# Kernel tuning notes

Hardware: AMD Instinct MI355X
Metric: run time of the kernel (lower is better)

The kernel has to match this reference:

```python
import jax, jax.numpy as jnp
import numpy as np

N = 20000      # number of nodes
K = 32         # neighbors per node (per edge type)
D_FEAT = 128   # feature dim


def setup_inputs() -> dict:
    key = jax.random.key(0)
    k1, k2, k3 = jax.random.split(key, 3)
    feat = jax.random.normal(k1, (N, D_FEAT), dtype=jnp.float32)
    sim_idx = jax.random.randint(k2, (N, K), 0, N)
    cor_idx = jax.random.randint(k3, (N, K), 0, N)
    return {"feat": feat, "sim_idx": sim_idx, "cor_idx": cor_idx}


def _coattention(Dm, Qm):
    # Dm, Qm: [N, K, d]
    L = jnp.einsum('nkd,njd->nkj', Dm, Qm)          # [N, K, K]
    AC = jax.nn.softmax(L, axis=-1)                  # softmax over Q-neighbors
    AS = jax.nn.softmax(jnp.swapaxes(L, 1, 2), axis=-1)  # softmax over D-neighbors
    CQ = jnp.einsum('nkj,njd->nkd', AC, Qm)          # [N, K, d]
    CD = jnp.einsum('nkj,njd->nkd', AS, jnp.concatenate([Dm, CQ], axis=-1))  # [N, K, 2d]
    return jnp.concatenate([Qm, CD], axis=-1)        # [N, K, 3d]


def reference(feat, sim_idx, cor_idx):
    # mode == 'cor': D <- sim edges, Q <- cor edges (dropout=0 => identity)
    Dm = feat[sim_idx]   # [N, K, d] gather
    Qm = feat[cor_idx]   # [N, K, d] gather
    h = _coattention(Dm, Qm)                          # [N, K, 3d]
    n, k, td = h.shape
    # AvgPool1d(kernel=3, stride=3) over last dim -> [N, K, d]
    h = h.reshape(n, k, td // 3, 3).mean(axis=-1)
    h_neigh = h.mean(axis=1)                          # mean over K neighbors -> [N, d]
    return feat + h_neigh
```

## Files before the change

### kernel.cpp

```cpp
#include <hip/hip_runtime.h>

#define KN 32
#define DF 128
#define WPB 2

typedef float  f32x16 __attribute__((ext_vector_type(16)));
typedef float  f32x2  __attribute__((ext_vector_type(2)));
typedef short  s16x8  __attribute__((ext_vector_type(8)));

union ldsu { int4 i; s16x8 v; };

__device__ __forceinline__ unsigned int pk_bf16(float lo, float hi) {
    unsigned int r;
    asm("v_cvt_pk_bf16_f32 %0, %1, %2" : "=v"(r) : "v"(lo), "v"(hi));
    return r;
}

__device__ __forceinline__ void gll16(const void* g, void* l) {
    __builtin_amdgcn_global_load_lds(
        (const __attribute__((address_space(1))) unsigned int*)g,
        (__attribute__((address_space(3))) unsigned int*)l,
        16, 0, 0);
}

__global__ __launch_bounds__(256)
void cvt_kernel(const float* __restrict__ f, unsigned short* __restrict__ bf,
                unsigned char* __restrict__ f8, int n8) {
    const int i = blockIdx.x * blockDim.x + threadIdx.x;
    if (i >= n8) return;
    float4 x0 = ((const float4*)f)[2 * i];
    float4 x1 = ((const float4*)f)[2 * i + 1];
    int4 b;
    b.x = (int)pk_bf16(x0.x, x0.y); b.y = (int)pk_bf16(x0.z, x0.w);
    b.z = (int)pk_bf16(x1.x, x1.y); b.w = (int)pk_bf16(x1.z, x1.w);
    ((int4*)bf)[i] = b;
    int p0 = __builtin_amdgcn_cvt_pk_fp8_f32(x0.x, x0.y, 0, false);
    p0     = __builtin_amdgcn_cvt_pk_fp8_f32(x0.z, x0.w, p0, true);
    int p1 = __builtin_amdgcn_cvt_pk_fp8_f32(x1.x, x1.y, 0, false);
    p1     = __builtin_amdgcn_cvt_pk_fp8_f32(x1.z, x1.w, p1, true);
    ((int2*)f8)[i] = make_int2(p0, p1);
}

__global__ __launch_bounds__(WPB * 64, 2)
void coattn_kernel(const float* __restrict__ feat,
                   const unsigned char* __restrict__ featbf,
                   const unsigned char* __restrict__ feat8,
                   const int* __restrict__ sim_idx,
                   const int* __restrict__ cor_idx,
                   float* __restrict__ out, int nnodes) {
    __shared__ int4 Ls[WPB][KN][8];
    const int wv = threadIdx.x >> 6;
    const int l  = threadIdx.x & 63;
    const int c  = l & 31;
    const int h  = l >> 5;
    const int g  = l >> 3;
    const int m  = l & 7;
    const int n  = blockIdx.x * WPB + wv;
    if (n >= nnodes) return;

    const int si = sim_idx[n * KN + c];
    const int ci = cor_idx[n * KN + c];
    const unsigned swz = (unsigned)(((m ^ g) & 7) * 16);

    f32x16 acc  = {0,0,0,0,0,0,0,0,0,0,0,0,0,0,0,0};
    f32x16 accT = {0,0,0,0,0,0,0,0,0,0,0,0,0,0,0,0};
    #pragma unroll
    for (int H = 0; H < 2; ++H) {
        const unsigned hoff = (unsigned)(H * 128) + swz;
        #pragma unroll
        for (int t = 0; t < 4; ++t) {
            const unsigned rD = (unsigned)__shfl(si, 8 * t + g, 64);
            gll16(featbf + rD * 256u + hoff, (void*)&Ls[wv][8 * t][0]);
        }
        asm volatile("s_waitcnt vmcnt(0)" ::: "memory");
        __builtin_amdgcn_sched_barrier(0);
        s16x8 fD[4];
        #pragma unroll
        for (int sp = 0; sp < 4; ++sp) {
            union ldsu u; u.i = Ls[wv][c][(sp * 2 + h) ^ (c & 7)];
            fD[sp] = u.v;
        }
        asm volatile("s_waitcnt lgkmcnt(0)" ::: "memory");
        __builtin_amdgcn_sched_barrier(0);
        #pragma unroll
        for (int t = 0; t < 4; ++t) {
            const unsigned rQ = (unsigned)__shfl(ci, 8 * t + g, 64);
            gll16(featbf + rQ * 256u + hoff, (void*)&Ls[wv][8 * t][0]);
        }
        asm volatile("s_waitcnt vmcnt(0)" ::: "memory");
        __builtin_amdgcn_sched_barrier(0);
        #pragma unroll
        for (int sp = 0; sp < 4; ++sp) {
            union ldsu uQ; uQ.i = Ls[wv][c][(sp * 2 + h) ^ (c & 7)];
            acc  = __builtin_amdgcn_mfma_f32_32x32x16_bf16(fD[sp], uQ.v, acc,  0, 0, 0);
            accT = __builtin_amdgcn_mfma_f32_32x32x16_bf16(uQ.v, fD[sp], accT, 0, 0, 0);
        }
        asm volatile("s_waitcnt lgkmcnt(0)" ::: "memory");
        __builtin_amdgcn_sched_barrier(0);
    }

    float mx = acc[0];
    #pragma unroll
    for (int p = 1; p < 16; ++p) mx = fmaxf(mx, acc[p]);
    mx = fmaxf(mx, __shfl_xor(mx, 32, 64));
    float z = 0.f;
    #pragma unroll
    for (int p = 0; p < 16; ++p) z += __expf(acc[p] - mx);
    z += __shfl_xor(z, 32, 64);
    const float invZ = 1.0f / z;

    float rm = accT[0];
    #pragma unroll
    for (int p = 1; p < 16; ++p) rm = fmaxf(rm, accT[p]);
    rm = fmaxf(rm, __shfl_xor(rm, 32, 64));
    float rs = 0.f;
    #pragma unroll
    for (int p = 0; p < 16; ++p) rs += __expf(accT[p] - rm);
    rs += __shfl_xor(rs, 32, 64);
    const float invR = 1.0f / rs;

    float w = 0.f;
    #pragma unroll
    for (int p = 0; p < 16; ++p) {
        const int jp = (p & 3) + 8 * (p >> 2) + 4 * h;
        w += __expf(accT[p] - __shfl(mx, jp, 64)) * __shfl(invZ, jp, 64);
    }
    w += __shfl_xor(w, 32, 64);

    const float u = w * invR;
    float v = 0.f;
    #pragma unroll
    for (int p = 0; p < 16; ++p) {
        const int kp = (p & 3) + 8 * (p >> 2) + 4 * h;
        v += __expf(acc[p] - __shfl(rm, kp, 64)) * __shfl(u, kp, 64);
    }
    v += __shfl_xor(v, 32, 64);

    float sQ[4] = {0,0,0,0}, sD[4] = {0,0,0,0}, sC[4] = {0,0,0,0};
    #pragma unroll
    for (int t = 0; t < 16; ++t) {
        const int b = h * 16 + t;
        const unsigned rD = (unsigned)__shfl(si, b, 64);
        const unsigned rQ = (unsigned)__shfl(ci, b, 64);
        const float wb = __shfl(w, b, 64);
        const float vb = __shfl(v, b, 64);
        const unsigned int da = *(const unsigned int*)(feat8 + (rD << 7) + 4u * c);
        const unsigned int dq = *(const unsigned int*)(feat8 + (rQ << 7) + 4u * c);
        f32x2 a01 = __builtin_amdgcn_cvt_pk_f32_fp8((int)da, false);
        f32x2 a23 = __builtin_amdgcn_cvt_pk_f32_fp8((int)da, true);
        f32x2 q01 = __builtin_amdgcn_cvt_pk_f32_fp8((int)dq, false);
        f32x2 q23 = __builtin_amdgcn_cvt_pk_f32_fp8((int)dq, true);
        sQ[0] += q01[0]; sQ[1] += q01[1]; sQ[2] += q23[0]; sQ[3] += q23[1];
        sD[0] = fmaf(wb, a01[0], sD[0]); sD[1] = fmaf(wb, a01[1], sD[1]);
        sD[2] = fmaf(wb, a23[0], sD[2]); sD[3] = fmaf(wb, a23[1], sD[3]);
        sC[0] = fmaf(vb, q01[0], sC[0]); sC[1] = fmaf(vb, q01[1], sC[1]);
        sC[2] = fmaf(vb, q23[0], sC[2]); sC[3] = fmaf(vb, q23[1], sC[3]);
    }
    #pragma unroll
    for (int i = 0; i < 4; ++i) {
        sQ[i] += __shfl_xor(sQ[i], 32, 64);
        sD[i] += __shfl_xor(sD[i], 32, 64);
        sC[i] += __shfl_xor(sC[i], 32, 64);
    }

    float* const S_sh = (float*)Ls[wv];
    if (h == 0) {
        *(float4*)&S_sh[0 * DF + 4 * c] = make_float4(sQ[0], sQ[1], sQ[2], sQ[3]);
        *(float4*)&S_sh[1 * DF + 4 * c] = make_float4(sD[0], sD[1], sD[2], sD[3]);
        *(float4*)&S_sh[2 * DF + 4 * c] = make_float4(sC[0], sC[1], sC[2], sC[3]);
    }
    asm volatile("s_waitcnt lgkmcnt(0)" ::: "memory");
    const float h0 = S_sh[6 * l + 0] + S_sh[6 * l + 1] + S_sh[6 * l + 2];
    const float h1 = S_sh[6 * l + 3] + S_sh[6 * l + 4] + S_sh[6 * l + 5];
    const float* fr = feat + (long)n * DF;
    const float o0 = fr[2 * l + 0] + h0 * (1.0f / 96.0f);
    const float o1 = fr[2 * l + 1] + h1 * (1.0f / 96.0f);
    *(float2*)&out[(long)n * DF + 2 * l] = make_float2(o0, o1);
}

#define RP 136
__global__ __launch_bounds__(64, 2)
void coattn_v4(const float* __restrict__ feat,
               const int* __restrict__ sim_idx,
               const int* __restrict__ cor_idx,
               float* __restrict__ out, int nnodes) {
    __shared__ unsigned char lds[2 * KN * RP];
    unsigned char* Ab8 = lds;
    unsigned char* Bb8 = lds + KN * RP;
    float* S_sh = (float*)lds;
    const int n = blockIdx.x;
    const int l = threadIdx.x;
    const int c = l & 31;
    const int h = l >> 5;
    const int si = sim_idx[n * KN + c];
    const int ci = cor_idx[n * KN + c];
    const float* Dr = feat + (long)si * DF;
    const float* Qr = feat + (long)ci * DF;
    f32x16 acc  = {0,0,0,0,0,0,0,0,0,0,0,0,0,0,0,0};
    f32x16 accT = {0,0,0,0,0,0,0,0,0,0,0,0,0,0,0,0};
    #pragma unroll
    for (int s = 0; s < 8; ++s) {
        const int d0 = s * 16 + h * 8;
        float4 a0 = *(const float4*)(Dr + d0);
        float4 a1 = *(const float4*)(Dr + d0 + 4);
        float4 b0 = *(const float4*)(Qr + d0);
        float4 b1 = *(const float4*)(Qr + d0 + 4);
        union { s16x8 v8; unsigned int u[4]; } ua, ub;
        ua.u[0] = pk_bf16(a0.x, a0.y); ua.u[1] = pk_bf16(a0.z, a0.w);
        ua.u[2] = pk_bf16(a1.x, a1.y); ua.u[3] = pk_bf16(a1.z, a1.w);
        ub.u[0] = pk_bf16(b0.x, b0.y); ub.u[1] = pk_bf16(b0.z, b0.w);
        ub.u[2] = pk_bf16(b1.x, b1.y); ub.u[3] = pk_bf16(b1.z, b1.w);
        acc  = __builtin_amdgcn_mfma_f32_32x32x16_bf16(ua.v8, ub.v8, acc,  0, 0, 0);
        accT = __builtin_amdgcn_mfma_f32_32x32x16_bf16(ub.v8, ua.v8, accT, 0, 0, 0);
        int pa0 = __builtin_amdgcn_cvt_pk_fp8_f32(a0.x, a0.y, 0, false);
        pa0     = __builtin_amdgcn_cvt_pk_fp8_f32(a0.z, a0.w, pa0, true);
        int pa1 = __builtin_amdgcn_cvt_pk_fp8_f32(a1.x, a1.y, 0, false);
        pa1     = __builtin_amdgcn_cvt_pk_fp8_f32(a1.z, a1.w, pa1, true);
        int pb0 = __builtin_amdgcn_cvt_pk_fp8_f32(b0.x, b0.y, 0, false);
        pb0     = __builtin_amdgcn_cvt_pk_fp8_f32(b0.z, b0.w, pb0, true);
        int pb1 = __builtin_amdgcn_cvt_pk_fp8_f32(b1.x, b1.y, 0, false);
        pb1     = __builtin_amdgcn_cvt_pk_fp8_f32(b1.z, b1.w, pb1, true);
        *(int2*)(Ab8 + c * RP + d0) = make_int2(pa0, pa1);
        *(int2*)(Bb8 + c * RP + d0) = make_int2(pb0, pb1);
    }
    float mx = acc[0];
    #pragma unroll
    for (int p = 1; p < 16; ++p) mx = fmaxf(mx, acc[p]);
    mx = fmaxf(mx, __shfl_xor(mx, 32, 64));
    float z = 0.f;
    #pragma unroll
    for (int p = 0; p < 16; ++p) z += __expf(acc[p] - mx);
    z += __shfl_xor(z, 32, 64);
    const float invZ = 1.0f / z;
    float rm = accT[0];
    #pragma unroll
    for (int p = 1; p < 16; ++p) rm = fmaxf(rm, accT[p]);
    rm = fmaxf(rm, __shfl_xor(rm, 32, 64));
    float rs = 0.f;
    #pragma unroll
    for (int p = 0; p < 16; ++p) rs += __expf(accT[p] - rm);
    rs += __shfl_xor(rs, 32, 64);
    const float invR = 1.0f / rs;
    float w = 0.f;
    #pragma unroll
    for (int p = 0; p < 16; ++p) {
        const int jp = (p & 3) + 8 * (p >> 2) + 4 * h;
        w += __expf(accT[p] - __shfl(mx, jp, 64)) * __shfl(invZ, jp, 64);
    }
    w += __shfl_xor(w, 32, 64);
    const float u = w * invR;
    float v = 0.f;
    #pragma unroll
    for (int p = 0; p < 16; ++p) {
        const int kp = (p & 3) + 8 * (p >> 2) + 4 * h;
        v += __expf(acc[p] - __shfl(rm, kp, 64)) * __shfl(u, kp, 64);
    }
    v += __shfl_xor(v, 32, 64);
    __syncthreads();
    float sQ[4] = {0,0,0,0}, sD[4] = {0,0,0,0}, sC[4] = {0,0,0,0};
    const unsigned char* Abase = Ab8 + h * 16 * RP + 4 * c;
    const unsigned char* Bbase = Bb8 + h * 16 * RP + 4 * c;
    #pragma unroll
    for (int t = 0; t < 16; ++t) {
        const int b = h * 16 + t;
        const float wb = __shfl(w, b, 64);
        const float vb = __shfl(v, b, 64);
        const unsigned int da = *(const unsigned int*)(Abase + t * RP);
        const unsigned int dq = *(const unsigned int*)(Bbase + t * RP);
        f32x2 a01 = __builtin_amdgcn_cvt_pk_f32_fp8((int)da, false);
        f32x2 a23 = __builtin_amdgcn_cvt_pk_f32_fp8((int)da, true);
        f32x2 q01 = __builtin_amdgcn_cvt_pk_f32_fp8((int)dq, false);
        f32x2 q23 = __builtin_amdgcn_cvt_pk_f32_fp8((int)dq, true);
        sQ[0] += q01[0]; sQ[1] += q01[1]; sQ[2] += q23[0]; sQ[3] += q23[1];
        sD[0] = fmaf(wb, a01[0], sD[0]); sD[1] = fmaf(wb, a01[1], sD[1]);
        sD[2] = fmaf(wb, a23[0], sD[2]); sD[3] = fmaf(wb, a23[1], sD[3]);
        sC[0] = fmaf(vb, q01[0], sC[0]); sC[1] = fmaf(vb, q01[1], sC[1]);
        sC[2] = fmaf(vb, q23[0], sC[2]);
        sC[3] = fmaf(vb, q23[1], sC[3]);
    }
    #pragma unroll
    for (int i = 0; i < 4; ++i) {
        sQ[i] += __shfl_xor(sQ[i], 32, 64);
        sD[i] += __shfl_xor(sD[i], 32, 64);
        sC[i] += __shfl_xor(sC[i], 32, 64);
    }
    __syncthreads();
    if (h == 0) {
        *(float4*)&S_sh[0 * DF + 4 * c] = make_float4(sQ[0], sQ[1], sQ[2], sQ[3]);
        *(float4*)&S_sh[1 * DF + 4 * c] = make_float4(sD[0], sD[1], sD[2], sD[3]);
        *(float4*)&S_sh[2 * DF + 4 * c] = make_float4(sC[0], sC[1], sC[2], sC[3]);
    }
    __syncthreads();
    const float h0 = S_sh[6 * l + 0] + S_sh[6 * l + 1] + S_sh[6 * l + 2];
    const float h1 = S_sh[6 * l + 3] + S_sh[6 * l + 4] + S_sh[6 * l + 5];
    const float* fr = feat + (long)n * DF;
    const float o0 = fr[2 * l + 0] + h0 * (1.0f / 96.0f);
    const float o1 = fr[2 * l + 1] + h1 * (1.0f / 96.0f);
    *(float2*)&out[(long)n * DF + 2 * l] = make_float2(o0, o1);
}

extern "C" void kernel_launch(void* const* d_in, const int* in_sizes, int n_in,
                              void* d_out, int out_size, void* d_ws, size_t ws_size,
                              hipStream_t stream) {
    const float* feat = (const float*)d_in[0];
    const int* sim    = (const int*)d_in[1];
    const int* cor    = (const int*)d_in[2];
    float* out        = (float*)d_out;
    const int nnodes  = in_sizes[0] / DF;
    const size_t nfeat = (size_t)nnodes * DF;
    const size_t need  = nfeat * 2 + nfeat;

    if (ws_size >= need) {
        unsigned short* featbf = (unsigned short*)d_ws;
        unsigned char*  feat8  = (unsigned char*)d_ws + nfeat * 2;
        const int n8 = (int)(nfeat / 8);
        hipLaunchKernelGGL(cvt_kernel, dim3((n8 + 255) / 256), dim3(256), 0, stream,
                           feat, featbf, feat8, n8);
        const int blocks = (nnodes + WPB - 1) / WPB;
        hipLaunchKernelGGL(coattn_kernel, dim3(blocks), dim3(WPB * 64), 0, stream,
                           feat, (const unsigned char*)featbf, feat8, sim, cor, out, nnodes);
    } else {
        hipLaunchKernelGGL(coattn_v4, dim3(nnodes), dim3(64), 0, stream,
                           feat, sim, cor, out, nnodes);
    }
}
```

Before: 61.91 us.

## Overlap D/Q and fp8 gathers with MFMA, fold log2e into bf16 scaling

The co-attention kernel now issues the D and Q bf16 gathers for both halves into separate LDS buffers, so the second half's loads and all fp8 row gathers for the final aggregation are in flight while the first half's MFMAs run. Fine-grained vmcnt waits replace the full drains that were needed before. The bf16 features are pre-scaled by sqrt(log2 e), so the MFMA logits come out in base-2 and the softmax can use raw v_exp_f32 instead of __expf. The aggregation FMAs are rewritten with 2-wide vectors to encourage packed math. The hand-counted vmcnt values and the extra registers held for 32 prefetched dwords add fragility and may raise register pressure.

```diff
diff --git a/kernel.cpp b/kernel.cpp
--- a/kernel.cpp
+++ b/kernel.cpp
@@ -15,7 +15,9 @@
     asm("v_cvt_pk_bf16_f32 %0, %1, %2" : "=v"(r) : "v"(lo), "v"(hi));
     return r;
 }
-
+__device__ __forceinline__ float ex2(float x) {
+    float r; asm("v_exp_f32 %0, %1" : "=v"(r) : "v"(x)); return r;
+}
 __device__ __forceinline__ void gll16(const void* g, void* l) {
     __builtin_amdgcn_global_load_lds(
         (const __attribute__((address_space(1))) unsigned int*)g,
@@ -28,11 +30,12 @@
                 unsigned char* __restrict__ f8, int n8) {
     const int i = blockIdx.x * blockDim.x + threadIdx.x;
     if (i >= n8) return;
+    const float s = 1.20112240872f;
     float4 x0 = ((const float4*)f)[2 * i];
     float4 x1 = ((const float4*)f)[2 * i + 1];
     int4 b;
-    b.x = (int)pk_bf16(x0.x, x0.y); b.y = (int)pk_bf16(x0.z, x0.w);
-    b.z = (int)pk_bf16(x1.x, x1.y); b.w = (int)pk_bf16(x1.z, x1.w);
+    b.x = (int)pk_bf16(s * x0.x, s * x0.y); b.y = (int)pk_bf16(s * x0.z, s * x0.w);
+    b.z = (int)pk_bf16(s * x1.x, s * x1.y); b.w = (int)pk_bf16(s * x1.z, s * x1.w);
     ((int4*)bf)[i] = b;
     int p0 = __builtin_amdgcn_cvt_pk_fp8_f32(x0.x, x0.y, 0, false);
     p0     = __builtin_amdgcn_cvt_pk_fp8_f32(x0.z, x0.w, p0, true);
@@ -48,7 +51,7 @@
                    const int* __restrict__ sim_idx,
                    const int* __restrict__ cor_idx,
                    float* __restrict__ out, int nnodes) {
-    __shared__ int4 Ls[WPB][KN][8];
+    __shared__ int4 Ls[WPB][2][KN][8];
     const int wv = threadIdx.x >> 6;
     const int l  = threadIdx.x & 63;
     const int c  = l & 31;
@@ -62,41 +65,79 @@
     const int ci = cor_idx[n * KN + c];
     const unsigned swz = (unsigned)(((m ^ g) & 7) * 16);
 
+    #pragma unroll
+    for (int t = 0; t < 4; ++t) {
+        const unsigned rD = (unsigned)__shfl(si, 8 * t + g, 64);
+        gll16(featbf + rD * 256u + swz, (void*)&Ls[wv][0][8 * t][0]);
+    }
+    #pragma unroll
+    for (int t = 0; t < 4; ++t) {
+        const unsigned rQ = (unsigned)__shfl(ci, 8 * t + g, 64);
+        gll16(featbf + rQ * 256u + swz, (void*)&Ls[wv][1][8 * t][0]);
+    }
+    asm volatile("s_waitcnt vmcnt(4)" ::: "memory");
+    __builtin_amdgcn_sched_barrier(0);
+    s16x8 fD[4], fQ[4];
+    #pragma unroll
+    for (int sp = 0; sp < 4; ++sp) {
+        union ldsu u; u.i = Ls[wv][0][c][(sp * 2 + h) ^ (c & 7)]; fD[sp] = u.v;
+    }
+    asm volatile("s_waitcnt vmcnt(0)" ::: "memory");
+    __builtin_amdgcn_sched_barrier(0);
+    #pragma unroll
+    for (int sp = 0; sp < 4; ++sp) {
+        union ldsu u; u.i = Ls[wv][1][c][(sp * 2 + h) ^ (c & 7)]; fQ[sp] = u.v;
+    }
+    asm volatile("s_waitcnt lgkmcnt(0)" ::: "memory");
+    __builtin_amdgcn_sched_barrier(0);
+
+    #pragma unroll
+    for (int t = 0; t < 4; ++t) {
+        const unsigned rD = (unsigned)__shfl(si, 8 * t + g, 64);
+        gll16(featbf + rD * 256u + 128u + swz, (void*)&Ls[wv][0][8 * t][0]);
+    }
+    #pragma unroll
+    for (int t = 0; t < 4; ++t) {
+        const unsigned rQ = (unsigned)__shfl(ci, 8 * t + g, 64);
+        gll16(featbf + rQ * 256u + 128u + swz, (void*)&Ls[wv][1][8 * t][0]);
+    }
+    unsigned int da[16], dq[16];
+    #pragma unroll
+    for (int t = 0; t < 16; ++t) {
+        const unsigned rD = (unsigned)__shfl(si, h * 16 + t, 64);
+        const unsigned rQ = (unsigned)__shfl(ci, h * 16 + t, 64);
+        const unsigned char* pD = feat8 + (rD << 7) + 4u * c;
+        const unsigned char* pQ = feat8 + (rQ << 7) + 4u * c;
+        asm volatile("global_load_dword %0, %1, off" : "=v"(da[t]) : "v"(pD) : "memory");
+        asm volatile("global_load_dword %0, %1, off" : "=v"(dq[t]) : "v"(pQ) : "memory");
+    }
+
     f32x16 acc  = {0,0,0,0,0,0,0,0,0,0,0,0,0,0,0,0};
     f32x16 accT = {0,0,0,0,0,0,0,0,0,0,0,0,0,0,0,0};
     #pragma unroll
-    for (int H = 0; H < 2; ++H) {
-        const unsigned hoff = (unsigned)(H * 128) + swz;
-        #pragma unroll
-        for (int t = 0; t < 4; ++t) {
-            const unsigned rD = (unsigned)__shfl(si, 8 * t + g, 64);
-            gll16(featbf + rD * 256u + hoff, (void*)&Ls[wv][8 * t][0]);
-        }
-        asm volatile("s_waitcnt vmcnt(0)" ::: "memory");
-        __builtin_amdgcn_sched_barrier(0);
-        s16x8 fD[4];
-        #pragma unroll
-        for (int sp = 0; sp < 4; ++sp) {
-            union ldsu u; u.i = Ls[wv][c][(sp * 2 + h) ^ (c & 7)];
-            fD[sp] = u.v;
-        }
-        asm volatile("s_waitcnt lgkmcnt(0)" ::: "memory");
-        __builtin_amdgcn_sched_barrier(0);
-        #pragma unroll
-        for (int t = 0; t < 4; ++t) {
-            const unsigned rQ = (unsigned)__shfl(ci, 8 * t + g, 64);
-            gll16(featbf + rQ * 256u + hoff, (void*)&Ls[wv][8 * t][0]);
-        }
-        asm volatile("s_waitcnt vmcnt(0)" ::: "memory");
-        __builtin_amdgcn_sched_barrier(0);
-        #pragma unroll
-        for (int sp = 0; sp < 4; ++sp) {
-            union ldsu uQ; uQ.i = Ls[wv][c][(sp * 2 + h) ^ (c & 7)];
-            acc  = __builtin_amdgcn_mfma_f32_32x32x16_bf16(fD[sp], uQ.v, acc,  0, 0, 0);
-            accT = __builtin_amdgcn_mfma_f32_32x32x16_bf16(uQ.v, fD[sp], accT, 0, 0, 0);
-        }
-        asm volatile("s_waitcnt lgkmcnt(0)" ::: "memory");
-        __builtin_amdgcn_sched_barrier(0);
+    for (int sp = 0; sp < 4; ++sp) {
+        acc  = __builtin_amdgcn_mfma_f32_32x32x16_bf16(fD[sp], fQ[sp], acc,  0, 0, 0);
+        accT = __builtin_amdgcn_mfma_f32_32x32x16_bf16(fQ[sp], fD[sp], accT, 0, 0, 0);
+    }
+
+    asm volatile("s_waitcnt vmcnt(36)" ::: "memory");
+    __builtin_amdgcn_sched_barrier(0);
+    #pragma unroll
+    for (int sp = 0; sp < 4; ++sp) {
+        union ldsu u; u.i = Ls[wv][0][c][(sp * 2 + h) ^ (c & 7)]; fD[sp] = u.v;
+    }
+    asm volatile("s_waitcnt vmcnt(32)" ::: "memory");
+    __builtin_amdgcn_sched_barrier(0);
+    #pragma unroll
+    for (int sp = 0; sp < 4; ++sp) {
+        union ldsu u; u.i = Ls[wv][1][c][(sp * 2 + h) ^ (c & 7)]; fQ[sp] = u.v;
+    }
+    asm volatile("s_waitcnt lgkmcnt(0)" ::: "memory");
+    __builtin_amdgcn_sched_barrier(0);
+    #pragma unroll
+    for (int sp = 0; sp < 4; ++sp) {
+        acc  = __builtin_amdgcn_mfma_f32_32x32x16_bf16(fD[sp], fQ[sp], acc,  0, 0, 0);
+        accT = __builtin_amdgcn_mfma_f32_32x32x16_bf16(fQ[sp], fD[sp], accT, 0, 0, 0);
     }
 
     float mx = acc[0];
@@ -105,7 +146,7 @@
     mx = fmaxf(mx, __shfl_xor(mx, 32, 64));
     float z = 0.f;
     #pragma unroll
-    for (int p = 0; p < 16; ++p) z += __expf(acc[p] - mx);
+    for (int p = 0; p < 16; ++p) z += ex2(acc[p] - mx);
     z += __shfl_xor(z, 32, 64);
     const float invZ = 1.0f / z;
 
@@ -115,7 +156,7 @@
     rm = fmaxf(rm, __shfl_xor(rm, 32, 64));
     float rs = 0.f;
     #pragma unroll
-    for (int p = 0; p < 16; ++p) rs += __expf(accT[p] - rm);
+    for (int p = 0; p < 16; ++p) rs += ex2(accT[p] - rm);
     rs += __shfl_xor(rs, 32, 64);
     const float invR = 1.0f / rs;
 
@@ -123,7 +164,7 @@
     #pragma unroll
     for (int p = 0; p < 16; ++p) {
         const int jp = (p & 3) + 8 * (p >> 2) + 4 * h;
-        w += __expf(accT[p] - __shfl(mx, jp, 64)) * __shfl(invZ, jp, 64);
+        w += ex2(accT[p] - __shfl(mx, jp, 64)) * __shfl(invZ, jp, 64);
     }
     w += __shfl_xor(w, 32, 64);
 
@@ -132,42 +173,42 @@
     #pragma unroll
     for (int p = 0; p < 16; ++p) {
         const int kp = (p & 3) + 8 * (p >> 2) + 4 * h;
-        v += __expf(acc[p] - __shfl(rm, kp, 64)) * __shfl(u, kp, 64);
+        v += ex2(acc[p] - __shfl(rm, kp, 64)) * __shfl(u, kp, 64);
     }
     v += __shfl_xor(v, 32, 64);
 
-    float sQ[4] = {0,0,0,0}, sD[4] = {0,0,0,0}, sC[4] = {0,0,0,0};
+    asm volatile("s_waitcnt vmcnt(0)" ::: "memory");
+    __builtin_amdgcn_sched_barrier(0);
+    f32x2 sQ2[2] = {{0.f,0.f},{0.f,0.f}};
+    f32x2 sD2[2] = {{0.f,0.f},{0.f,0.f}};
+    f32x2 sC2[2] = {{0.f,0.f},{0.f,0.f}};
     #pragma unroll
     for (int t = 0; t < 16; ++t) {
         const int b = h * 16 + t;
-        const unsigned rD = (unsigned)__shfl(si, b, 64);
-        const unsigned rQ = (unsigned)__shfl(ci, b, 64);
         const float wb = __shfl(w, b, 64);
         const float vb = __shfl(v, b, 64);
-        const unsigned int da = *(const unsigned int*)(feat8 + (rD << 7) + 4u * c);
-        const unsigned int dq = *(const unsigned int*)(feat8 + (rQ << 7) + 4u * c);
-        f32x2 a01 = __builtin_amdgcn_cvt_pk_f32_fp8((int)da, false);
-        f32x2 a23 = __builtin_amdgcn_cvt_pk_f32_fp8((int)da, true);
-        f32x2 q01 = __builtin_amdgcn_cvt_pk_f32_fp8((int)dq, false);
-        f32x2 q23 = __builtin_amdgcn_cvt_pk_f32_fp8((int)dq, true);
-        sQ[0] += q01[0]; sQ[1] += q01[1]; sQ[2] += q23[0]; sQ[3] += q23[1];
-        sD[0] = fmaf(wb, a01[0], sD[0]); sD[1] = fmaf(wb, a01[1], sD[1]);
-        sD[2] = fmaf(wb, a23[0], sD[2]); sD[3] = fmaf(wb, a23[1], sD[3]);
-        sC[0] = fmaf(vb, q01[0], sC[0]); sC[1] = fmaf(vb, q01[1], sC[1]);
-        sC[2] = fmaf(vb, q23[0], sC[2]); sC[3] = fmaf(vb, q23[1], sC[3]);
-    }
-    #pragma unroll
-    for (int i = 0; i < 4; ++i) {
-        sQ[i] += __shfl_xor(sQ[i], 32, 64);
-        sD[i] += __shfl_xor(sD[i], 32, 64);
-        sC[i] += __shfl_xor(sC[i], 32, 64);
+        f32x2 a01 = __builtin_amdgcn_cvt_pk_f32_fp8((int)da[t], false);
+        f32x2 a23 = __builtin_amdgcn_cvt_pk_f32_fp8((int)da[t], true);
+        f32x2 q01 = __builtin_amdgcn_cvt_pk_f32_fp8((int)dq[t], false);
+        f32x2 q23 = __builtin_amdgcn_cvt_pk_f32_fp8((int)dq[t], true);
+        const f32x2 wb2 = {wb, wb};
+        const f32x2 vb2 = {vb, vb};
+        sQ2[0] += q01;                sQ2[1] += q23;
+        sD2[0] = wb2 * a01 + sD2[0];  sD2[1] = wb2 * a23 + sD2[1];
+        sC2[0] = vb2 * q01 + sC2[0];  sC2[1] = vb2 * q23 + sC2[1];
+    }
+    #pragma unroll
+    for (int i = 0; i < 2; ++i) {
+        sQ2[i][0] += __shfl_xor(sQ2[i][0], 32, 64); sQ2[i][1] += __shfl_xor(sQ2[i][1], 32, 64);
+        sD2[i][0] += __shfl_xor(sD2[i][0], 32, 64); sD2[i][1] += __shfl_xor(sD2[i][1], 32, 64);
+        sC2[i][0] += __shfl_xor(sC2[i][0], 32, 64); sC2[i][1] += __shfl_xor(sC2[i][1], 32, 64);
     }
 
     float* const S_sh = (float*)Ls[wv];
     if (h == 0) {
-        *(float4*)&S_sh[0 * DF + 4 * c] = make_float4(sQ[0], sQ[1], sQ[2], sQ[3]);
-        *(float4*)&S_sh[1 * DF + 4 * c] = make_float4(sD[0], sD[1], sD[2], sD[3]);
-        *(float4*)&S_sh[2 * DF + 4 * c] = make_float4(sC[0], sC[1], sC[2], sC[3]);
+        *(float4*)&S_sh[0 * DF + 4 * c] = make_float4(sQ2[0][0], sQ2[0][1], sQ2[1][0], sQ2[1][1]);
+        *(float4*)&S_sh[1 * DF + 4 * c] = make_float4(sD2[0][0], sD2[0][1], sD2[1][0], sD2[1][1]);
+        *(float4*)&S_sh[2 * DF + 4 * c] = make_float4(sC2[0][0], sC2[0][1], sC2[1][0], sC2[1][1]);
     }
     asm volatile("s_waitcnt lgkmcnt(0)" ::: "memory");
     const float h0 = S_sh[6 * l + 0] + S_sh[6 * l + 1] + S_sh[6 * l + 2];
```

Measured after the change: 63.99 us. 3.4% more time.

## Reuse staged bf16 rows for pooling, prefetch all halves, fold log2e into scaling

Applied to the files above, without the earlier changes.

The conversion kernel now writes only a bf16 copy, pre-scaled by sqrt(log2 e), so the raw v_exp_f32 base-2 instruction can compute softmax exponentials directly. The coattention kernel issues all four D/Q half-row gathers into a larger LDS buffer up front, so the second half's loads overlap the first half's MFMAs. The weighted neighbor sums then read the bf16 rows already in LDS instead of doing a second global gather of an fp8 copy. Output is rescaled by 1/s to compensate. The cost is four times the LDS per block and the extra scaling multiplies.

```diff
diff --git a/kernel.cpp b/kernel.cpp
--- a/kernel.cpp
+++ b/kernel.cpp
@@ -5,7 +5,6 @@
 #define WPB 2
 
 typedef float  f32x16 __attribute__((ext_vector_type(16)));
-typedef float  f32x2  __attribute__((ext_vector_type(2)));
 typedef short  s16x8  __attribute__((ext_vector_type(8)));
 
 union ldsu { int4 i; s16x8 v; };
@@ -15,6 +14,11 @@
     asm("v_cvt_pk_bf16_f32 %0, %1, %2" : "=v"(r) : "v"(lo), "v"(hi));
     return r;
 }
+__device__ __forceinline__ float ex2(float x) {
+    float r; asm("v_exp_f32 %0, %1" : "=v"(r) : "v"(x)); return r;
+}
+__device__ __forceinline__ float bflo(unsigned int u) { return __uint_as_float(u << 16); }
+__device__ __forceinline__ float bfhi(unsigned int u) { return __uint_as_float(u & 0xffff0000u); }
 
 __device__ __forceinline__ void gll16(const void* g, void* l) {
     __builtin_amdgcn_global_load_lds(
@@ -24,31 +28,25 @@
 }
 
 __global__ __launch_bounds__(256)
-void cvt_kernel(const float* __restrict__ f, unsigned short* __restrict__ bf,
-                unsigned char* __restrict__ f8, int n8) {
+void cvt_kernel(const float* __restrict__ f, unsigned short* __restrict__ bf, int n8) {
     const int i = blockIdx.x * blockDim.x + threadIdx.x;
     if (i >= n8) return;
+    const float s = 1.20112240872f;
     float4 x0 = ((const float4*)f)[2 * i];
     float4 x1 = ((const float4*)f)[2 * i + 1];
     int4 b;
-    b.x = (int)pk_bf16(x0.x, x0.y); b.y = (int)pk_bf16(x0.z, x0.w);
-    b.z = (int)pk_bf16(x1.x, x1.y); b.w = (int)pk_bf16(x1.z, x1.w);
+    b.x = (int)pk_bf16(s * x0.x, s * x0.y); b.y = (int)pk_bf16(s * x0.z, s * x0.w);
+    b.z = (int)pk_bf16(s * x1.x, s * x1.y); b.w = (int)pk_bf16(s * x1.z, s * x1.w);
     ((int4*)bf)[i] = b;
-    int p0 = __builtin_amdgcn_cvt_pk_fp8_f32(x0.x, x0.y, 0, false);
-    p0     = __builtin_amdgcn_cvt_pk_fp8_f32(x0.z, x0.w, p0, true);
-    int p1 = __builtin_amdgcn_cvt_pk_fp8_f32(x1.x, x1.y, 0, false);
-    p1     = __builtin_amdgcn_cvt_pk_fp8_f32(x1.z, x1.w, p1, true);
-    ((int2*)f8)[i] = make_int2(p0, p1);
 }
 
 __global__ __launch_bounds__(WPB * 64, 2)
 void coattn_kernel(const float* __restrict__ feat,
                    const unsigned char* __restrict__ featbf,
-                   const unsigned char* __restrict__ feat8,
                    const int* __restrict__ sim_idx,
                    const int* __restrict__ cor_idx,
                    float* __restrict__ out, int nnodes) {
-    __shared__ int4 Ls[WPB][KN][8];
+    __shared__ int4 Ls[WPB][2][2][KN][8];
     const int wv = threadIdx.x >> 6;
     const int l  = threadIdx.x & 63;
     const int c  = l & 31;
@@ -62,41 +60,57 @@
     const int ci = cor_idx[n * KN + c];
     const unsigned swz = (unsigned)(((m ^ g) & 7) * 16);
 
+    #pragma unroll
+    for (int t = 0; t < 4; ++t) {
+        const unsigned rD = (unsigned)__shfl(si, 8 * t + g, 64);
+        gll16(featbf + rD * 256u + swz, (void*)&Ls[wv][0][0][8 * t][0]);
+    }
+    #pragma unroll
+    for (int t = 0; t < 4; ++t) {
+        const unsigned rQ = (unsigned)__shfl(ci, 8 * t + g, 64);
+        gll16(featbf + rQ * 256u + swz, (void*)&Ls[wv][1][0][8 * t][0]);
+    }
+    #pragma unroll
+    for (int t = 0; t < 4; ++t) {
+        const unsigned rD = (unsigned)__shfl(si, 8 * t + g, 64);
+        gll16(featbf + rD * 256u + 128u + swz, (void*)&Ls[wv][0][1][8 * t][0]);
+    }
+    #pragma unroll
+    for (int t = 0; t < 4; ++t) {
+        const unsigned rQ = (unsigned)__shfl(ci, 8 * t + g, 64);
+        gll16(featbf + rQ * 256u + 128u + swz, (void*)&Ls[wv][1][1][8 * t][0]);
+    }
+
     f32x16 acc  = {0,0,0,0,0,0,0,0,0,0,0,0,0,0,0,0};
     f32x16 accT = {0,0,0,0,0,0,0,0,0,0,0,0,0,0,0,0};
-    #pragma unroll
-    for (int H = 0; H < 2; ++H) {
-        const unsigned hoff = (unsigned)(H * 128) + swz;
-        #pragma unroll
-        for (int t = 0; t < 4; ++t) {
-            const unsigned rD = (unsigned)__shfl(si, 8 * t + g, 64);
-            gll16(featbf + rD * 256u + hoff, (void*)&Ls[wv][8 * t][0]);
-        }
-        asm volatile("s_waitcnt vmcnt(0)" ::: "memory");
-        __builtin_amdgcn_sched_barrier(0);
-        s16x8 fD[4];
-        #pragma unroll
-        for (int sp = 0; sp < 4; ++sp) {
-            union ldsu u; u.i = Ls[wv][c][(sp * 2 + h) ^ (c & 7)];
-            fD[sp] = u.v;
-        }
-        asm volatile("s_waitcnt lgkmcnt(0)" ::: "memory");
-        __builtin_amdgcn_sched_barrier(0);
-        #pragma unroll
-        for (int t = 0; t < 4; ++t) {
-            const unsigned rQ = (unsigned)__shfl(ci, 8 * t + g, 64);
-            gll16(featbf + rQ * 256u + hoff, (void*)&Ls[wv][8 * t][0]);
-        }
-        asm volatile("s_waitcnt vmcnt(0)" ::: "memory");
-        __builtin_amdgcn_sched_barrier(0);
-        #pragma unroll
-        for (int sp = 0; sp < 4; ++sp) {
-            union ldsu uQ; uQ.i = Ls[wv][c][(sp * 2 + h) ^ (c & 7)];
-            acc  = __builtin_amdgcn_mfma_f32_32x32x16_bf16(fD[sp], uQ.v, acc,  0, 0, 0);
-            accT = __builtin_amdgcn_mfma_f32_32x32x16_bf16(uQ.v, fD[sp], accT, 0, 0, 0);
-        }
-        asm volatile("s_waitcnt lgkmcnt(0)" ::: "memory");
-        __builtin_amdgcn_sched_barrier(0);
+    asm volatile("s_waitcnt vmcnt(8)" ::: "memory");
+    __builtin_amdgcn_sched_barrier(0);
+    s16x8 fD[4], fQ[4];
+    #pragma unroll
+    for (int sp = 0; sp < 4; ++sp) {
+        union ldsu uD, uQ;
+        uD.i = Ls[wv][0][0][c][(sp * 2 + h) ^ (c & 7)];
+        uQ.i = Ls[wv][1][0][c][(sp * 2 + h) ^ (c & 7)];
+        fD[sp] = uD.v; fQ[sp] = uQ.v;
+    }
+    #pragma unroll
+    for (int sp = 0; sp < 4; ++sp) {
+        acc  = __builtin_amdgcn_mfma_f32_32x32x16_bf16(fD[sp], fQ[sp], acc,  0, 0, 0);
+        accT = __builtin_amdgcn_mfma_f32_32x32x16_bf16(fQ[sp], fD[sp], accT, 0, 0, 0);
+    }
+    asm volatile("s_waitcnt vmcnt(0)" ::: "memory");
+    __builtin_amdgcn_sched_barrier(0);
+    #pragma unroll
+    for (int sp = 0; sp < 4; ++sp) {
+        union ldsu uD, uQ;
+        uD.i = Ls[wv][0][1][c][(sp * 2 + h) ^ (c & 7)];
+        uQ.i = Ls[wv][1][1][c][(sp * 2 + h) ^ (c & 7)];
+        fD[sp] = uD.v; fQ[sp] = uQ.v;
+    }
+    #pragma unroll
+    for (int sp = 0; sp < 4; ++sp) {
+        acc  = __builtin_amdgcn_mfma_f32_32x32x16_bf16(fD[sp], fQ[sp], acc,  0, 0, 0);
+        accT = __builtin_amdgcn_mfma_f32_32x32x16_bf16(fQ[sp], fD[sp], accT, 0, 0, 0);
     }
 
     float mx = acc[0];
@@ -105,7 +119,7 @@
     mx = fmaxf(mx, __shfl_xor(mx, 32, 64));
     float z = 0.f;
     #pragma unroll
-    for (int p = 0; p < 16; ++p) z += __expf(acc[p] - mx);
+    for (int p = 0; p < 16; ++p) z += ex2(acc[p] - mx);
     z += __shfl_xor(z, 32, 64);
     const float invZ = 1.0f / z;
 
@@ -115,7 +129,7 @@
     rm = fmaxf(rm, __shfl_xor(rm, 32, 64));
     float rs = 0.f;
     #pragma unroll
-    for (int p = 0; p < 16; ++p) rs += __expf(accT[p] - rm);
+    for (int p = 0; p < 16; ++p) rs += ex2(accT[p] - rm);
     rs += __shfl_xor(rs, 32, 64);
     const float invR = 1.0f / rs;
 
@@ -123,7 +137,7 @@
     #pragma unroll
     for (int p = 0; p < 16; ++p) {
         const int jp = (p & 3) + 8 * (p >> 2) + 4 * h;
-        w += __expf(accT[p] - __shfl(mx, jp, 64)) * __shfl(invZ, jp, 64);
+        w += ex2(accT[p] - __shfl(mx, jp, 64)) * __shfl(invZ, jp, 64);
     }
     w += __shfl_xor(w, 32, 64);
 
@@ -132,29 +146,31 @@
     #pragma unroll
     for (int p = 0; p < 16; ++p) {
         const int kp = (p & 3) + 8 * (p >> 2) + 4 * h;
-        v += __expf(acc[p] - __shfl(rm, kp, 64)) * __shfl(u, kp, 64);
+        v += ex2(acc[p] - __shfl(rm, kp, 64)) * __shfl(u, kp, 64);
     }
     v += __shfl_xor(v, 32, 64);
 
     float sQ[4] = {0,0,0,0}, sD[4] = {0,0,0,0}, sC[4] = {0,0,0,0};
+    const int hf = c >> 4;
+    const int cb = (c >> 1) & 7;
+    const int bo = (c & 1) * 8;
     #pragma unroll
     for (int t = 0; t < 16; ++t) {
         const int b = h * 16 + t;
-        const unsigned rD = (unsigned)__shfl(si, b, 64);
-        const unsigned rQ = (unsigned)__shfl(ci, b, 64);
         const float wb = __shfl(w, b, 64);
         const float vb = __shfl(v, b, 64);
-        const unsigned int da = *(const unsigned int*)(feat8 + (rD << 7) + 4u * c);
-        const unsigned int dq = *(const unsigned int*)(feat8 + (rQ << 7) + 4u * c);
-        f32x2 a01 = __builtin_amdgcn_cvt_pk_f32_fp8((int)da, false);
-        f32x2 a23 = __builtin_amdgcn_cvt_pk_f32_fp8((int)da, true);
-        f32x2 q01 = __builtin_amdgcn_cvt_pk_f32_fp8((int)dq, false);
-        f32x2 q23 = __builtin_amdgcn_cvt_pk_f32_fp8((int)dq, true);
-        sQ[0] += q01[0]; sQ[1] += q01[1]; sQ[2] += q23[0]; sQ[3] += q23[1];
-        sD[0] = fmaf(wb, a01[0], sD[0]); sD[1] = fmaf(wb, a01[1], sD[1]);
-        sD[2] = fmaf(wb, a23[0], sD[2]); sD[3] = fmaf(wb, a23[1], sD[3]);
-        sC[0] = fmaf(vb, q01[0], sC[0]); sC[1] = fmaf(vb, q01[1], sC[1]);
-        sC[2] = fmaf(vb, q23[0], sC[2]); sC[3] = fmaf(vb, q23[1], sC[3]);
+        const int ch = cb ^ (b & 7);
+        const int2 dd = *(const int2*)((const char*)&Ls[wv][0][hf][b][ch] + bo);
+        const int2 qq = *(const int2*)((const char*)&Ls[wv][1][hf][b][ch] + bo);
+        const float a0 = bflo((unsigned)dd.x), a1 = bfhi((unsigned)dd.x);
+        const float a2 = bflo((unsigned)dd.y), a3 = bfhi((unsigned)dd.y);
+        const float q0 = bflo((unsigned)qq.x), q1 = bfhi((unsigned)qq.x);
+        const float q2 = bflo((unsigned)qq.y), q3 = bfhi((unsigned)qq.y);
+        sQ[0] += q0; sQ[1] += q1; sQ[2] += q2; sQ[3] += q3;
+        sD[0] = fmaf(wb, a0, sD[0]); sD[1] = fmaf(wb, a1, sD[1]);
+        sD[2] = fmaf(wb, a2, sD[2]); sD[3] = fmaf(wb, a3, sD[3]);
+        sC[0] = fmaf(vb, q0, sC[0]); sC[1] = fmaf(vb, q1, sC[1]);
+        sC[2] = fmaf(vb, q2, sC[2]); sC[3] = fmaf(vb, q3, sC[3]);
     }
     #pragma unroll
     for (int i = 0; i < 4; ++i) {
@@ -164,21 +180,25 @@
     }
 
     float* const S_sh = (float*)Ls[wv];
+    asm volatile("s_waitcnt lgkmcnt(0)" ::: "memory");
+    __builtin_amdgcn_sched_barrier(0);
     if (h == 0) {
         *(float4*)&S_sh[0 * DF + 4 * c] = make_float4(sQ[0], sQ[1], sQ[2], sQ[3]);
         *(float4*)&S_sh[1 * DF + 4 * c] = make_float4(sD[0], sD[1], sD[2], sD[3]);
         *(float4*)&S_sh[2 * DF + 4 * c] = make_float4(sC[0], sC[1], sC[2], sC[3]);
     }
     asm volatile("s_waitcnt lgkmcnt(0)" ::: "memory");
+    const float k = (1.0f / 96.0f) * (1.0f / 1.20112240872f);
     const float h0 = S_sh[6 * l + 0] + S_sh[6 * l + 1] + S_sh[6 * l + 2];
     const float h1 = S_sh[6 * l + 3] + S_sh[6 * l + 4] + S_sh[6 * l + 5];
     const float* fr = feat + (long)n * DF;
-    const float o0 = fr[2 * l + 0] + h0 * (1.0f / 96.0f);
-    const float o1 = fr[2 * l + 1] + h1 * (1.0f / 96.0f);
+    const float o0 = fr[2 * l + 0] + h0 * k;
+    const float o1 = fr[2 * l + 1] + h1 * k;
     *(float2*)&out[(long)n * DF + 2 * l] = make_float2(o0, o1);
 }
 
 #define RP 136
+typedef float f32x2 __attribute__((ext_vector_type(2)));
 __global__ __launch_bounds__(64, 2)
 void coattn_v4(const float* __restrict__ feat,
                const int* __restrict__ sim_idx,
@@ -308,17 +328,16 @@
     float* out        = (float*)d_out;
     const int nnodes  = in_sizes[0] / DF;
     const size_t nfeat = (size_t)nnodes * DF;
-    const size_t need  = nfeat * 2 + nfeat;
+    const size_t need  = nfeat * 2;
 
     if (ws_size >= need) {
         unsigned short* featbf = (unsigned short*)d_ws;
-        unsigned char*  feat8  = (unsigned char*)d_ws + nfeat * 2;
         const int n8 = (int)(nfeat / 8);
         hipLaunchKernelGGL(cvt_kernel, dim3((n8 + 255) / 256), dim3(256), 0, stream,
-                           feat, featbf, feat8, n8);
+                           feat, featbf, n8);
         const int blocks = (nnodes + WPB - 1) / WPB;
         hipLaunchKernelGGL(coattn_kernel, dim3(blocks), dim3(WPB * 64), 0, stream,
-                           feat, (const unsigned char*)featbf, feat8, sim, cor, out, nnodes);
+                           feat, (const unsigned char*)featbf, sim, cor, out, nnodes);
     } else {
         hipLaunchKernelGGL(coattn_v4, dim3(nnodes), dim3(64), 0, stream,
                            feat, sim, cor, out, nnodes);
```

After: 68.22 us. 1.1x slower.
